# Performance work log

Measured on AMD Instinct MI355X. Metric: run time of the kernel, lower is better.

Reference implementation:

```python
import jax, jax.numpy as jnp
import numpy as np

N = 20000      # nodes
E = 640000     # edges
F = 128        # input features
H = 256        # hidden dim
G = 64         # graphs in batch


def setup_inputs() -> dict:
    key = jax.random.key(0)
    ks = jax.random.split(key, 24)
    w = lambda k, sh: (jax.random.normal(k, sh, jnp.float32) * 0.05)
    inp = {
        'x': jax.random.normal(ks[0], (N, F), jnp.float32),
        'edge_index': jax.random.randint(ks[1], (2, E), 0, N, dtype=jnp.int32),
        'batch': jnp.sort(jax.random.randint(ks[2], (N,), 0, G, dtype=jnp.int32)),
        # GCN stack
        'gcn_w1': w(ks[3], (F, H)), 'gcn_b1': jnp.zeros((H,), jnp.float32),
        'gcn_w2': w(ks[4], (H, H)), 'gcn_b2': jnp.zeros((H,), jnp.float32),
        'gcn_w3': w(ks[5], (H, H)), 'gcn_b3': jnp.zeros((H,), jnp.float32),
        'gcn_w4': w(ks[6], (H, H)), 'gcn_b4': jnp.zeros((H,), jnp.float32),
        # EdgeConv 1: Linear(2F,H) -> ReLU -> Linear(H,H)
        'ec1_w1': w(ks[7], (2 * F, H)), 'ec1_b1': jnp.zeros((H,), jnp.float32),
        'ec1_w2': w(ks[8], (H, H)),     'ec1_b2': jnp.zeros((H,), jnp.float32),
        # EdgeConv 2: Linear(2H,H) -> ReLU -> Linear(H,H)
        'ec2_w1': w(ks[9], (2 * H, H)), 'ec2_b1': jnp.zeros((H,), jnp.float32),
        'ec2_w2': w(ks[10], (H, H)),    'ec2_b2': jnp.zeros((H,), jnp.float32),
        # head
        'fc1_w': w(ks[11], (2 * H, H)), 'fc1_b': jnp.zeros((H,), jnp.float32),
        'out_w': w(ks[12], (H, 1)),     'out_b': jnp.zeros((1,), jnp.float32),
    }
    return inp


def _gcn_conv(x, W, b, src, dst, n):
    # PyG GCNConv: add self loops, symmetric deg^-1/2 normalization, scatter-sum.
    h = x @ W                                        # [n, H]
    loops = jnp.arange(n, dtype=src.dtype)
    s = jnp.concatenate([src, loops])
    d = jnp.concatenate([dst, loops])
    deg = jax.ops.segment_sum(jnp.ones(s.shape[0], x.dtype), d, num_segments=n)
    dinv = jnp.where(deg > 0, jax.lax.rsqrt(deg), 0.0)
    norm = (dinv[s] * dinv[d])[:, None]              # [E+n, 1]
    return jax.ops.segment_sum(h[s] * norm, d, num_segments=n) + b


def _edge_conv(x, w1, b1, w2, b2, src, dst, n):
    # PyG EdgeConv: msg = MLP([x_i, x_j - x_i]), max-aggregate at target i.
    xi = x[dst]
    xj = x[src]
    m = jnp.concatenate([xi, xj - xi], axis=1)       # [E, 2*d]
    m = jax.nn.relu(m @ w1 + b1) @ w2 + b2           # [E, H]
    out = jax.ops.segment_max(m, dst, num_segments=n)
    return jnp.where(jnp.isfinite(out), out, 0.0)    # empty segments -> 0


def reference(x, edge_index, batch,
              gcn_w1, gcn_b1, gcn_w2, gcn_b2, gcn_w3, gcn_b3, gcn_w4, gcn_b4,
              ec1_w1, ec1_b1, ec1_w2, ec1_b2, ec2_w1, ec2_b1, ec2_w2, ec2_b2,
              fc1_w, fc1_b, out_w, out_b):
    n = x.shape[0]
    src, dst = edge_index[0], edge_index[1]
    relu = jax.nn.relu
    # GCN branch (dropout is identity at inference)
    xg = relu(_gcn_conv(x, gcn_w1, gcn_b1, src, dst, n))
    xg = relu(_gcn_conv(xg, gcn_w2, gcn_b2, src, dst, n))
    xg = relu(_gcn_conv(xg, gcn_w3, gcn_b3, src, dst, n))
    xg = relu(_gcn_conv(xg, gcn_w4, gcn_b4, src, dst, n))
    # EdgeConv branch
    xe = relu(_edge_conv(x, ec1_w1, ec1_b1, ec1_w2, ec1_b2, src, dst, n))
    xe = relu(_edge_conv(xe, ec2_w1, ec2_b1, ec2_w2, ec2_b2, src, dst, n))
    # pool per graph + head
    x_cat = jnp.concatenate([xg, xe], axis=1)        # [n, 512]
    g = jax.ops.segment_sum(x_cat, batch, num_segments=G)  # [G, 512]
    g = relu(g @ fc1_w + fc1_b)
    return g @ out_w + out_b                          # [G, 1]
```

## Files before the change

kernel.cpp:

```cpp
#include <hip/hip_runtime.h>

#define HD 256

typedef __attribute__((ext_vector_type(8))) __bf16 bf16x8;
typedef __attribute__((ext_vector_type(4))) __bf16 bf16x4;
typedef __attribute__((ext_vector_type(4))) float f32x4;

static __device__ __forceinline__ float relu_f(float x){ return x > 0.f ? x : 0.f; }

static __device__ __forceinline__ void split4(const float* m, bf16x4& vh, bf16x4& vl){
    #pragma unroll
    for (int j = 0; j < 4; j++){
        float v = m[j];
        __bf16 h = (__bf16)v;
        vh[j] = h;
        vl[j] = (__bf16)(v - (float)h);
    }
}

__global__ void k_count(const int* __restrict__ dst, int* __restrict__ cnt, int E){
    int i = blockIdx.x * blockDim.x + threadIdx.x;
    if (i < E) atomicAdd(&cnt[dst[i]], 1);
}

__global__ void k_scan(const int* __restrict__ cnt, int* __restrict__ row_ptr,
                       float* __restrict__ dinv, int n){
    __shared__ int lds[1024];
    int t = threadIdx.x;
    int carry = 0;
    for (int base = 0; base < n; base += 1024){
        int idx = base + t;
        int v = (idx < n) ? cnt[idx] : 0;
        if (idx < n) dinv[idx] = 1.0f / sqrtf((float)(v + 1));
        __syncthreads();
        lds[t] = v;
        __syncthreads();
        for (int off = 1; off < 1024; off <<= 1){
            int add = (t >= off) ? lds[t - off] : 0;
            __syncthreads();
            lds[t] += add;
            __syncthreads();
        }
        int incl = lds[t];
        if (idx < n) row_ptr[idx] = carry + incl - v;
        carry += lds[1023];
    }
    if (t == 0) row_ptr[n] = carry;
}

__global__ void k_fill(const int* __restrict__ src, const int* __restrict__ dst,
                       const int* __restrict__ row_ptr, int* __restrict__ fill,
                       int* __restrict__ csr_src, int* __restrict__ csr_dst, int E){
    int i = blockIdx.x * blockDim.x + threadIdx.x;
    if (i < E){
        int d = dst[i];
        int pos = row_ptr[d] + atomicAdd(&fill[d], 1);
        csr_src[pos] = src[i];
        csr_dst[pos] = d;
    }
}

struct PackDesc { const float* src; const float* src2; __bf16* ph; __bf16* pl; int K; int pad; };
struct PackArgs { PackDesc d[10]; };

__global__ void k_wpack_all(PackArgs a){
    PackDesc p = a.d[blockIdx.y];
    int total = (p.K >> 5) * 8192;
    int idx = blockIdx.x * 256 + threadIdx.x;
    if (idx >= total) return;
    int j = idx & 7, g = (idx >> 3) & 3, c = (idx >> 5) & 255, ks = idx >> 13;
    int k = ks * 32 + g * 8 + j;
    float v = p.src[(size_t)k * HD + c];
    if (p.src2) v -= p.src2[(size_t)k * HD + c];
    __bf16 h = (__bf16)v;
    p.ph[idx] = h;
    p.pl[idx] = (__bf16)(v - (float)h);
}

template<int KS>
__global__ __launch_bounds__(512, 4) void k_gemm_mfma(
    const float* __restrict__ A,
    const __bf16* __restrict__ Wph, const __bf16* __restrict__ Wpl,
    const float* __restrict__ bias,
    float* __restrict__ C, int M, int K)
{
    __shared__ __bf16 mh[2][64][40];
    __shared__ __bf16 ml[2][64][40];
    int t = threadIdx.x;
    int m0 = blockIdx.x * 64;
    const int w = t >> 6, fr = t & 15, fg = (t & 63) >> 4;
    const int srow = t >> 3, skb = (t & 7) * 4;
    int ar = m0 + srow; if (ar >= M) ar = M - 1;
    const float* Arow = A + (size_t)ar * K + skb;
    const int c0 = w * 32 + fr;

    auto stage = [&](int buf, const float4& a){
        float m4[4] = {a.x, a.y, a.z, a.w};
        bf16x4 vh, vl;
        split4(m4, vh, vl);
        *(bf16x4*)&mh[buf][srow][skb] = vh;
        *(bf16x4*)&ml[buf][srow][skb] = vl;
    };

    f32x4 acc[4][2];
    #pragma unroll
    for (int i = 0; i < 4; i++)
        #pragma unroll
        for (int j = 0; j < 2; j++) acc[i][j] = (f32x4){0.f, 0.f, 0.f, 0.f};

    float4 rA[KS];
    #pragma unroll
    for (int c = 0; c < KS; c++) rA[c] = *(const float4*)(Arow + c * 32);

    stage(0, rA[0]);

    #pragma unroll
    for (int ks = 0; ks < KS; ++ks){
        bf16x8 bh[2], bl[2];
        #pragma unroll
        for (int nf = 0; nf < 2; nf++){
            size_t bi = ((size_t)(ks * 256 + c0 + nf * 16) * 4 + fg) * 8;
            bh[nf] = *(const bf16x8*)(Wph + bi);
            bl[nf] = *(const bf16x8*)(Wpl + bi);
        }
        __syncthreads();
        const int cb = ks & 1;
        #pragma unroll
        for (int mf = 0; mf < 4; mf++){
            bf16x8 ah = *(const bf16x8*)&mh[cb][mf * 16 + fr][fg * 8];
            bf16x8 al = *(const bf16x8*)&ml[cb][mf * 16 + fr][fg * 8];
            #pragma unroll
            for (int nf = 0; nf < 2; nf++){
                acc[mf][nf] = __builtin_amdgcn_mfma_f32_16x16x32_bf16(ah, bh[nf], acc[mf][nf], 0, 0, 0);
                acc[mf][nf] = __builtin_amdgcn_mfma_f32_16x16x32_bf16(al, bh[nf], acc[mf][nf], 0, 0, 0);
                acc[mf][nf] = __builtin_amdgcn_mfma_f32_16x16x32_bf16(ah, bl[nf], acc[mf][nf], 0, 0, 0);
            }
        }
        if (ks + 1 < KS) stage(cb ^ 1, rA[ks + 1]);
    }

    float bj[2];
    #pragma unroll
    for (int nf = 0; nf < 2; nf++) bj[nf] = bias ? bias[c0 + nf * 16] : 0.f;
    #pragma unroll
    for (int mf = 0; mf < 4; mf++)
        #pragma unroll
        for (int reg = 0; reg < 4; reg++){
            int row = m0 + mf * 16 + fg * 4 + reg;
            if (row < M){
                #pragma unroll
                for (int nf = 0; nf < 2; nf++)
                    C[(size_t)row * HD + c0 + nf * 16] = acc[mf][nf][reg] + bj[nf];
            }
        }
}

__global__ __launch_bounds__(256) void k_gcn_agg(const float* __restrict__ h,
                                                 const float* __restrict__ dinv,
                                                 const int* __restrict__ row_ptr,
                                                 const int* __restrict__ csr_src,
                                                 const float* __restrict__ bias,
                                                 float* __restrict__ out, int n){
    int wid = threadIdx.x >> 6, lane = threadIdx.x & 63;
    int i = blockIdx.x * 4 + wid;
    if (i >= n) return;
    float di = dinv[i];
    const float4* hp = (const float4*)h;
    float4 v = hp[(size_t)i * 64 + lane];
    float ax0 = v.x * di, ay0 = v.y * di, az0 = v.z * di, aw0 = v.w * di;
    float ax1 = 0.f, ay1 = 0.f, az1 = 0.f, aw1 = 0.f;
    float ax2 = 0.f, ay2 = 0.f, az2 = 0.f, aw2 = 0.f;
    float ax3 = 0.f, ay3 = 0.f, az3 = 0.f, aw3 = 0.f;
    int e0 = row_ptr[i], e1 = row_ptr[i + 1];
    int e = e0;
    for (; e + 3 < e1; e += 4){
        int s0 = csr_src[e], s1 = csr_src[e + 1], s2 = csr_src[e + 2], s3 = csr_src[e + 3];
        float q0 = dinv[s0], q1 = dinv[s1], q2 = dinv[s2], q3 = dinv[s3];
        float4 u0 = hp[(size_t)s0 * 64 + lane];
        float4 u1 = hp[(size_t)s1 * 64 + lane];
        float4 u2 = hp[(size_t)s2 * 64 + lane];
        float4 u3 = hp[(size_t)s3 * 64 + lane];
        ax0 += u0.x * q0; ay0 += u0.y * q0; az0 += u0.z * q0; aw0 += u0.w * q0;
        ax1 += u1.x * q1; ay1 += u1.y * q1; az1 += u1.z * q1; aw1 += u1.w * q1;
        ax2 += u2.x * q2; ay2 += u2.y * q2; az2 += u2.z * q2; aw2 += u2.w * q2;
        ax3 += u3.x * q3; ay3 += u3.y * q3; az3 += u3.z * q3; aw3 += u3.w * q3;
    }
    for (; e < e1; e++){
        int s = csr_src[e];
        float q = dinv[s];
        float4 u = hp[(size_t)s * 64 + lane];
        ax0 += u.x * q; ay0 += u.y * q; az0 += u.z * q; aw0 += u.w * q;
    }
    float ax = (ax0 + ax1) + (ax2 + ax3);
    float ay = (ay0 + ay1) + (ay2 + ay3);
    float az = (az0 + az1) + (az2 + az3);
    float aw = (aw0 + aw1) + (aw2 + aw3);
    const float4 b = ((const float4*)bias)[lane];
    float4 o;
    o.x = relu_f(ax * di + b.x);
    o.y = relu_f(ay * di + b.y);
    o.z = relu_f(az * di + b.z);
    o.w = relu_f(aw * di + b.w);
    ((float4*)out)[(size_t)i * 64 + lane] = o;
}

__global__ __launch_bounds__(512, 4) void k_edge_mfma(
    const float* __restrict__ A, const float* __restrict__ B,
    const __bf16* __restrict__ Wph, const __bf16* __restrict__ Wpl,
    const float* __restrict__ bias,
    const int* __restrict__ csr_src, const int* __restrict__ csr_dst,
    float* __restrict__ out, int E)
{
    __shared__ __bf16 mh[2][64][40];
    __shared__ __bf16 ml[2][64][40];
    __shared__ int sdst[64], ssrc[64];
    int t = threadIdx.x;
    int nwg = gridDim.x;
    int q = nwg >> 3, r = nwg & 7;
    int xc = blockIdx.x & 7;
    int bid = (xc < r ? xc * (q + 1) : r * (q + 1) + (xc - r) * q) + (blockIdx.x >> 3);
    int p0 = bid * 64;
    if (t < 64){
        int e = p0 + t; if (e >= E) e = E - 1;
        sdst[t] = csr_dst[e];
        ssrc[t] = csr_src[e];
    }
    __syncthreads();

    const int w  = t >> 6;
    const int fr = t & 15;
    const int fg = (t & 63) >> 4;
    const int srow = t >> 3, skb = (t & 7) * 4;
    const float* Arow = A + (size_t)sdst[srow] * HD + skb;
    const float* Brow = B + (size_t)ssrc[srow] * HD + skb;
    const int c0 = w * 32 + fr;

    auto stage = [&](int buf, const float4& a, const float4& g){
        float m4[4] = {relu_f(a.x + g.x), relu_f(a.y + g.y), relu_f(a.z + g.z), relu_f(a.w + g.w)};
        bf16x4 vh, vl;
        split4(m4, vh, vl);
        *(bf16x4*)&mh[buf][srow][skb] = vh;
        *(bf16x4*)&ml[buf][srow][skb] = vl;
    };

    f32x4 acc[4][2];
    #pragma unroll
    for (int i = 0; i < 4; i++)
        #pragma unroll
        for (int j = 0; j < 2; j++) acc[i][j] = (f32x4){0.f, 0.f, 0.f, 0.f};

    float4 ra[4], rg[4];
    #pragma unroll
    for (int c = 0; c < 4; c++){
        ra[c] = *(const float4*)(Arow + c * 32);
        rg[c] = *(const float4*)(Brow + c * 32);
    }
    stage(0, ra[0], rg[0]);

    #pragma unroll
    for (int ks = 0; ks < 8; ++ks){
        if (ks + 4 < 8){
            ra[ks & 3] = *(const float4*)(Arow + (ks + 4) * 32);
            rg[ks & 3] = *(const float4*)(Brow + (ks + 4) * 32);
        }
        bf16x8 bh[2], bl[2];
        #pragma unroll
        for (int nf = 0; nf < 2; nf++){
            size_t bi = ((size_t)(ks * 256 + c0 + nf * 16) * 4 + fg) * 8;
            bh[nf] = *(const bf16x8*)(Wph + bi);
            bl[nf] = *(const bf16x8*)(Wpl + bi);
        }
        __syncthreads();
        const int cb = ks & 1;
        #pragma unroll
        for (int mf = 0; mf < 4; mf++){
            bf16x8 ah = *(const bf16x8*)&mh[cb][mf * 16 + fr][fg * 8];
            bf16x8 al = *(const bf16x8*)&ml[cb][mf * 16 + fr][fg * 8];
            #pragma unroll
            for (int nf = 0; nf < 2; nf++){
                acc[mf][nf] = __builtin_amdgcn_mfma_f32_16x16x32_bf16(ah, bh[nf], acc[mf][nf], 0, 0, 0);
                acc[mf][nf] = __builtin_amdgcn_mfma_f32_16x16x32_bf16(al, bh[nf], acc[mf][nf], 0, 0, 0);
                acc[mf][nf] = __builtin_amdgcn_mfma_f32_16x16x32_bf16(ah, bl[nf], acc[mf][nf], 0, 0, 0);
            }
        }
        if (ks < 7) stage(cb ^ 1, ra[(ks + 1) & 3], rg[(ks + 1) & 3]);
    }

    float bj[2];
    #pragma unroll
    for (int nf = 0; nf < 2; nf++) bj[nf] = bias[c0 + nf * 16];
    int curd = sdst[fg * 4];
    float v[2];
    #pragma unroll
    for (int nf = 0; nf < 2; nf++) v[nf] = acc[0][nf][0] + bj[nf];
    #pragma unroll
    for (int mf = 0; mf < 4; mf++){
        #pragma unroll
        for (int reg = 0; reg < 4; reg++){
            if (mf == 0 && reg == 0) continue;
            int d = sdst[mf * 16 + fg * 4 + reg];
            if (d != curd){
                #pragma unroll
                for (int nf = 0; nf < 2; nf++)
                    if (v[nf] > 0.f)
                        atomicMax((int*)(out + (size_t)curd * HD + c0 + nf * 16), __float_as_int(v[nf]));
                curd = d;
                #pragma unroll
                for (int nf = 0; nf < 2; nf++) v[nf] = acc[mf][nf][reg] + bj[nf];
            } else {
                #pragma unroll
                for (int nf = 0; nf < 2; nf++) v[nf] = fmaxf(v[nf], acc[mf][nf][reg] + bj[nf]);
            }
        }
    }
    #pragma unroll
    for (int nf = 0; nf < 2; nf++)
        if (v[nf] > 0.f)
            atomicMax((int*)(out + (size_t)curd * HD + c0 + nf * 16), __float_as_int(v[nf]));
}

__global__ __launch_bounds__(512) void k_pool_head(const float* __restrict__ xg,
                                                   const float* __restrict__ xe,
                                                   const int* __restrict__ batch,
                                                   const float* __restrict__ w1,
                                                   const float* __restrict__ b1,
                                                   const float* __restrict__ w2,
                                                   const float* __restrict__ b2,
                                                   float* __restrict__ out, int n){
    __shared__ float gp[512];
    __shared__ float red[256];
    int g = blockIdx.x, t = threadIdx.x;
    int lo, hi;
    { int l = 0, h = n; while (l < h){ int m = (l + h) >> 1; if (batch[m] < g) l = m + 1; else h = m; } lo = l; }
    { int l = lo, h = n; while (l < h){ int m = (l + h) >> 1; if (batch[m] < g + 1) l = m + 1; else h = m; } hi = l; }
    const float* sp = (t < 256) ? (xg + t) : (xe + (t - 256));
    float a0 = 0.f, a1 = 0.f;
    int i = lo;
    for (; i + 1 < hi; i += 2){
        a0 += sp[(size_t)i * HD];
        a1 += sp[(size_t)(i + 1) * HD];
    }
    if (i < hi) a0 += sp[(size_t)i * HD];
    gp[t] = a0 + a1;
    __syncthreads();
    if (t < 256){
        float acc = b1[t];
        #pragma unroll 4
        for (int k = 0; k < 512; k++) acc += gp[k] * w1[k * HD + t];
        red[t] = relu_f(acc) * w2[t];
    }
    __syncthreads();
    for (int s = 128; s > 0; s >>= 1){
        if (t < s) red[t] += red[t + s];
        __syncthreads();
    }
    if (t == 0) out[g] = red[0] + b2[0];
}

extern "C" void kernel_launch(void* const* d_in, const int* in_sizes, int n_in,
                              void* d_out, int out_size, void* d_ws, size_t ws_size,
                              hipStream_t stream){
    const float* x      = (const float*)d_in[0];
    const int*   ei     = (const int*)d_in[1];
    const int*   batch  = (const int*)d_in[2];
    const float* gcn_w[4] = {(const float*)d_in[3], (const float*)d_in[5], (const float*)d_in[7], (const float*)d_in[9]};
    const float* gcn_b[4] = {(const float*)d_in[4], (const float*)d_in[6], (const float*)d_in[8], (const float*)d_in[10]};
    const float* ec1_w1 = (const float*)d_in[11]; const float* ec1_b1 = (const float*)d_in[12];
    const float* ec1_w2 = (const float*)d_in[13]; const float* ec1_b2 = (const float*)d_in[14];
    const float* ec2_w1 = (const float*)d_in[15]; const float* ec2_b1 = (const float*)d_in[16];
    const float* ec2_w2 = (const float*)d_in[17]; const float* ec2_b2 = (const float*)d_in[18];
    const float* fc1_w  = (const float*)d_in[19]; const float* fc1_b  = (const float*)d_in[20];
    const float* out_w  = (const float*)d_in[21]; const float* out_b  = (const float*)d_in[22];

    const int N = in_sizes[2];
    const int E = in_sizes[1] / 2;
    const int F = in_sizes[0] / N;
    const int* src = ei;
    const int* dst = ei + E;
    const int GB64 = (N + 63) / 64;
    const int EB   = (E + 63) / 64;

    char* w = (char*)d_ws;
    auto alloc = [&](size_t bytes) -> char* {
        char* p = w;
        w += (bytes + 255) & ~(size_t)255;
        return p;
    };
    int*   cnt     = (int*)alloc((size_t)N * 4);
    int*   fillc   = (int*)alloc((size_t)N * 4);
    int*   row_ptr = (int*)alloc((size_t)(N + 1) * 4);
    int*   csr_src = (int*)alloc((size_t)E * 4);
    int*   csr_dst = (int*)alloc((size_t)E * 4);
    float* dinv    = (float*)alloc((size_t)N * 4);
    float* act     = (float*)alloc((size_t)N * HD * 4);
    float* hbuf    = (float*)alloc((size_t)N * HD * 4);
    float* Bbuf    = (float*)alloc((size_t)N * HD * 4);
    float* xebuf   = (float*)alloc((size_t)N * HD * 4);
    auto packa = [&](int K) -> __bf16* { return (__bf16*)alloc((size_t)K * 256 * 2); };
    __bf16* pg1h = packa(128); __bf16* pg1l = packa(128);
    __bf16* pg2h = packa(256); __bf16* pg2l = packa(256);
    __bf16* pg3h = packa(256); __bf16* pg3l = packa(256);
    __bf16* pg4h = packa(256); __bf16* pg4l = packa(256);
    __bf16* pe1ah = packa(128); __bf16* pe1al = packa(128);
    __bf16* pe1bh = packa(128); __bf16* pe1bl = packa(128);
    __bf16* pe2ah = packa(256); __bf16* pe2al = packa(256);
    __bf16* pe2bh = packa(256); __bf16* pe2bl = packa(256);
    __bf16* w2h1 = packa(256); __bf16* w2l1 = packa(256);
    __bf16* w2h2 = packa(256); __bf16* w2l2 = packa(256);

    hipMemsetAsync(cnt, 0, (size_t)N * 4, stream);
    hipMemsetAsync(fillc, 0, (size_t)N * 4, stream);
    k_count<<<(E + 255) / 256, 256, 0, stream>>>(dst, cnt, E);
    k_scan<<<1, 1024, 0, stream>>>(cnt, row_ptr, dinv, N);
    k_fill<<<(E + 255) / 256, 256, 0, stream>>>(src, dst, row_ptr, fillc, csr_src, csr_dst, E);

    PackArgs pa;
    pa.d[0] = {gcn_w[0],                  nullptr,                    pg1h,  pg1l,  F,  0};
    pa.d[1] = {gcn_w[1],                  nullptr,                    pg2h,  pg2l,  HD, 0};
    pa.d[2] = {gcn_w[2],                  nullptr,                    pg3h,  pg3l,  HD, 0};
    pa.d[3] = {gcn_w[3],                  nullptr,                    pg4h,  pg4l,  HD, 0};
    pa.d[4] = {ec1_w1,                    ec1_w1 + (size_t)F * HD,    pe1ah, pe1al, F,  0};
    pa.d[5] = {ec1_w1 + (size_t)F * HD,   nullptr,                    pe1bh, pe1bl, F,  0};
    pa.d[6] = {ec2_w1,                    ec2_w1 + (size_t)HD * HD,   pe2ah, pe2al, HD, 0};
    pa.d[7] = {ec2_w1 + (size_t)HD * HD,  nullptr,                    pe2bh, pe2bl, HD, 0};
    pa.d[8] = {ec1_w2,                    nullptr,                    w2h1,  w2l1,  HD, 0};
    pa.d[9] = {ec2_w2,                    nullptr,                    w2h2,  w2l2,  HD, 0};
    k_wpack_all<<<dim3(256, 10), 256, 0, stream>>>(pa);

    k_gemm_mfma<4><<<GB64, 512, 0, stream>>>(x, pg1h, pg1l, nullptr, hbuf, N, F);
    k_gcn_agg<<<(N + 3) / 4, 256, 0, stream>>>(hbuf, dinv, row_ptr, csr_src, gcn_b[0], act, N);
    const __bf16* pgh[3] = {pg2h, pg3h, pg4h};
    const __bf16* pgl[3] = {pg2l, pg3l, pg4l};
    for (int l = 0; l < 3; l++){
        k_gemm_mfma<8><<<GB64, 512, 0, stream>>>(act, pgh[l], pgl[l], nullptr, hbuf, N, HD);
        k_gcn_agg<<<(N + 3) / 4, 256, 0, stream>>>(hbuf, dinv, row_ptr, csr_src, gcn_b[l + 1], act, N);
    }

    k_gemm_mfma<4><<<GB64, 512, 0, stream>>>(x, pe1ah, pe1al, ec1_b1, hbuf, N, F);
    k_gemm_mfma<4><<<GB64, 512, 0, stream>>>(x, pe1bh, pe1bl, nullptr, Bbuf, N, F);
    hipMemsetAsync(xebuf, 0, (size_t)N * HD * 4, stream);
    k_edge_mfma<<<EB, 512, 0, stream>>>(hbuf, Bbuf, w2h1, w2l1, ec1_b2, csr_src, csr_dst, xebuf, E);

    k_gemm_mfma<8><<<GB64, 512, 0, stream>>>(xebuf, pe2ah, pe2al, ec2_b1, hbuf, N, HD);
    k_gemm_mfma<8><<<GB64, 512, 0, stream>>>(xebuf, pe2bh, pe2bl, nullptr, Bbuf, N, HD);
    hipMemsetAsync(xebuf, 0, (size_t)N * HD * 4, stream);
    k_edge_mfma<<<EB, 512, 0, stream>>>(hbuf, Bbuf, w2h2, w2l2, ec2_b2, csr_src, csr_dst, xebuf, E);

    k_pool_head<<<64, 512, 0, stream>>>(act, xebuf, batch, fc1_w, fc1_b, out_w, out_b, (float*)d_out, N);
}
```

Before: 1.341 ms.

## Fuse paired EdgeConv input GEMMs into one dual-output kernel; shrink edge prefetch depth

Adds a dual GEMM kernel in which two wave groups share one staged bf16-split tile of A and each computes a different weight matrix into its own output. The two back-to-back GEMMs over the same input in each EdgeConv layer become one launch. This removes a second read and split of A and one launch. Separately, the edge MFMA kernel drops its 4-deep register prefetch of gathered rows in favour of a single-step lookahead and removes the unroll pragma, to cut register pressure at the cost of less load latency hiding. Each wave in the dual kernel now holds 16 accumulators, which may lower occupancy.

```diff
diff --git a/kernel.cpp b/kernel.cpp
--- a/kernel.cpp
+++ b/kernel.cpp
@@ -150,6 +150,88 @@
             if (row < M){
                 #pragma unroll
                 for (int nf = 0; nf < 2; nf++)
+                    C[(size_t)row * HD + c0 + nf * 16] = acc[mf][nf][reg] + bj[nf];
+            }
+        }
+}
+
+template<int KS>
+__global__ __launch_bounds__(512, 4) void k_gemm_mfma_dual(
+    const float* __restrict__ A,
+    const __bf16* __restrict__ Wph1, const __bf16* __restrict__ Wpl1,
+    const float* __restrict__ bias1, float* __restrict__ C1,
+    const __bf16* __restrict__ Wph2, const __bf16* __restrict__ Wpl2,
+    float* __restrict__ C2, int M, int K)
+{
+    __shared__ __bf16 mh[2][64][40];
+    __shared__ __bf16 ml[2][64][40];
+    int t = threadIdx.x;
+    int m0 = blockIdx.x * 64;
+    const int w = t >> 6, grp = w >> 2, wl = w & 3;
+    const int fr = t & 15, fg = (t & 63) >> 4;
+    const int srow = t >> 3, skb = (t & 7) * 4;
+    int ar = m0 + srow; if (ar >= M) ar = M - 1;
+    const float* Arow = A + (size_t)ar * K + skb;
+    const int c0 = wl * 64 + fr;
+    const __bf16* Wph = grp ? Wph2 : Wph1;
+    const __bf16* Wpl = grp ? Wpl2 : Wpl1;
+    float* C = grp ? C2 : C1;
+
+    auto stage = [&](int buf, const float4& a){
+        float m4[4] = {a.x, a.y, a.z, a.w};
+        bf16x4 vh, vl;
+        split4(m4, vh, vl);
+        *(bf16x4*)&mh[buf][srow][skb] = vh;
+        *(bf16x4*)&ml[buf][srow][skb] = vl;
+    };
+
+    f32x4 acc[4][4];
+    #pragma unroll
+    for (int i = 0; i < 4; i++)
+        #pragma unroll
+        for (int j = 0; j < 4; j++) acc[i][j] = (f32x4){0.f, 0.f, 0.f, 0.f};
+
+    float4 ra[2];
+    ra[0] = *(const float4*)(Arow);
+    stage(0, ra[0]);
+
+    #pragma unroll
+    for (int ks = 0; ks < KS; ++ks){
+        if (ks + 1 < KS) ra[(ks + 1) & 1] = *(const float4*)(Arow + (ks + 1) * 32);
+        bf16x8 bh[4], bl[4];
+        #pragma unroll
+        for (int nf = 0; nf < 4; nf++){
+            size_t bi = ((size_t)(ks * 256 + c0 + nf * 16) * 4 + fg) * 8;
+            bh[nf] = *(const bf16x8*)(Wph + bi);
+            bl[nf] = *(const bf16x8*)(Wpl + bi);
+        }
+        __syncthreads();
+        const int cb = ks & 1;
+        #pragma unroll
+        for (int mf = 0; mf < 4; mf++){
+            bf16x8 ah = *(const bf16x8*)&mh[cb][mf * 16 + fr][fg * 8];
+            bf16x8 al = *(const bf16x8*)&ml[cb][mf * 16 + fr][fg * 8];
+            #pragma unroll
+            for (int nf = 0; nf < 4; nf++){
+                acc[mf][nf] = __builtin_amdgcn_mfma_f32_16x16x32_bf16(ah, bh[nf], acc[mf][nf], 0, 0, 0);
+                acc[mf][nf] = __builtin_amdgcn_mfma_f32_16x16x32_bf16(al, bh[nf], acc[mf][nf], 0, 0, 0);
+                acc[mf][nf] = __builtin_amdgcn_mfma_f32_16x16x32_bf16(ah, bl[nf], acc[mf][nf], 0, 0, 0);
+            }
+        }
+        if (ks + 1 < KS) stage(cb ^ 1, ra[(ks + 1) & 1]);
+    }
+
+    float bj[4];
+    #pragma unroll
+    for (int nf = 0; nf < 4; nf++) bj[nf] = grp ? 0.f : bias1[c0 + nf * 16];
+    #pragma unroll
+    for (int mf = 0; mf < 4; mf++)
+        #pragma unroll
+        for (int reg = 0; reg < 4; reg++){
+            int row = m0 + mf * 16 + fg * 4 + reg;
+            if (row < M){
+                #pragma unroll
+                for (int nf = 0; nf < 4; nf++)
                     C[(size_t)row * HD + c0 + nf * 16] = acc[mf][nf][reg] + bj[nf];
             }
         }
@@ -249,19 +331,17 @@
         #pragma unroll
         for (int j = 0; j < 2; j++) acc[i][j] = (f32x4){0.f, 0.f, 0.f, 0.f};
 
-    float4 ra[4], rg[4];
-    #pragma unroll
-    for (int c = 0; c < 4; c++){
-        ra[c] = *(const float4*)(Arow + c * 32);
-        rg[c] = *(const float4*)(Brow + c * 32);
-    }
-    stage(0, ra[0], rg[0]);
-
-    #pragma unroll
+    {
+        float4 a = *(const float4*)(Arow);
+        float4 g = *(const float4*)(Brow);
+        stage(0, a, g);
+    }
+
     for (int ks = 0; ks < 8; ++ks){
-        if (ks + 4 < 8){
-            ra[ks & 3] = *(const float4*)(Arow + (ks + 4) * 32);
-            rg[ks & 3] = *(const float4*)(Brow + (ks + 4) * 32);
+        float4 a, g;
+        if (ks < 7){
+            a = *(const float4*)(Arow + (ks + 1) * 32);
+            g = *(const float4*)(Brow + (ks + 1) * 32);
         }
         bf16x8 bh[2], bl[2];
         #pragma unroll
@@ -283,7 +363,7 @@
                 acc[mf][nf] = __builtin_amdgcn_mfma_f32_16x16x32_bf16(ah, bl[nf], acc[mf][nf], 0, 0, 0);
             }
         }
-        if (ks < 7) stage(cb ^ 1, ra[(ks + 1) & 3], rg[(ks + 1) & 3]);
+        if (ks < 7) stage(cb ^ 1, a, g);
     }
 
     float bj[2];
@@ -436,13 +516,13 @@
         k_gcn_agg<<<(N + 3) / 4, 256, 0, stream>>>(hbuf, dinv, row_ptr, csr_src, gcn_b[l + 1], act, N);
     }
 
-    k_gemm_mfma<4><<<GB64, 512, 0, stream>>>(x, pe1ah, pe1al, ec1_b1, hbuf, N, F);
-    k_gemm_mfma<4><<<GB64, 512, 0, stream>>>(x, pe1bh, pe1bl, nullptr, Bbuf, N, F);
+    k_gemm_mfma_dual<4><<<GB64, 512, 0, stream>>>(x, pe1ah, pe1al, ec1_b1, hbuf,
+                                                  pe1bh, pe1bl, Bbuf, N, F);
     hipMemsetAsync(xebuf, 0, (size_t)N * HD * 4, stream);
     k_edge_mfma<<<EB, 512, 0, stream>>>(hbuf, Bbuf, w2h1, w2l1, ec1_b2, csr_src, csr_dst, xebuf, E);
 
-    k_gemm_mfma<8><<<GB64, 512, 0, stream>>>(xebuf, pe2ah, pe2al, ec2_b1, hbuf, N, HD);
-    k_gemm_mfma<8><<<GB64, 512, 0, stream>>>(xebuf, pe2bh, pe2bl, nullptr, Bbuf, N, HD);
+    k_gemm_mfma_dual<8><<<GB64, 512, 0, stream>>>(xebuf, pe2ah, pe2al, ec2_b1, hbuf,
+                                                  pe2bh, pe2bl, Bbuf, N, HD);
     hipMemsetAsync(xebuf, 0, (size_t)N * HD * 4, stream);
     k_edge_mfma<<<EB, 512, 0, stream>>>(hbuf, Bbuf, w2h2, w2l2, ec2_b2, csr_src, csr_dst, xebuf, E);
 
```

Result: faster. 1.279 ms (-4.6%).
